# Optimization experiments

Measured on AMD Instinct MI355X. Metric: run time of the kernel, lower is better.

Reference implementation:

```python
import jax, jax.numpy as jnp
import numpy as np

B, T, I = 16384, 101, 4
H = 512  # lstm_hidden_layer_size
M = 512  # mlp_hidden_layer_size


def setup_inputs() -> dict:
    key = jax.random.key(0)
    ks = jax.random.split(key, 10)
    s_ih = 1.0 / np.sqrt(H)
    inp = {
        "batch_x": jax.random.normal(ks[0], (B, T, I), dtype=jnp.float32),
        "batch_a": jax.random.uniform(ks[1], (B, 1), dtype=jnp.float32),
        # PyTorch nn.LSTM params (gate order i,f,g,o), U(-1/sqrt(H), 1/sqrt(H))
        "W_ih": jax.random.uniform(ks[2], (4 * H, I), minval=-s_ih, maxval=s_ih, dtype=jnp.float32),
        "W_hh": jax.random.uniform(ks[3], (4 * H, H), minval=-s_ih, maxval=s_ih, dtype=jnp.float32),
        "b_ih": jax.random.uniform(ks[4], (4 * H,), minval=-s_ih, maxval=s_ih, dtype=jnp.float32),
        "b_hh": jax.random.uniform(ks[5], (4 * H,), minval=-s_ih, maxval=s_ih, dtype=jnp.float32),
        "W1": jax.random.uniform(ks[6], (M, H), minval=-s_ih, maxval=s_ih, dtype=jnp.float32),
        "b1": jax.random.uniform(ks[7], (M,), minval=-s_ih, maxval=s_ih, dtype=jnp.float32),
        "W2": jax.random.uniform(ks[8], (1, M + 1), minval=-1.0 / np.sqrt(M + 1), maxval=1.0 / np.sqrt(M + 1), dtype=jnp.float32),
        "b2": jax.random.uniform(ks[9], (1,), minval=-1.0 / np.sqrt(M + 1), maxval=1.0 / np.sqrt(M + 1), dtype=jnp.float32),
    }
    return inp


def _lstm_last_hidden(batch_x, W_ih, W_hh, b_ih, b_hh):
    h = W_hh.shape[1]
    # input projections for all timesteps at once: [T, B, 4H]
    x_proj = jnp.einsum("bti,gi->tbg", batch_x, W_ih) + b_ih + b_hh

    def step(carry, xp):
        h_t, c_t = carry
        gates = xp + h_t @ W_hh.T  # [B, 4H]
        i, f, g, o = jnp.split(gates, 4, axis=-1)
        i = jax.nn.sigmoid(i)
        f = jax.nn.sigmoid(f)
        g = jnp.tanh(g)
        o = jax.nn.sigmoid(o)
        c_new = f * c_t + i * g
        h_new = o * jnp.tanh(c_new)
        return (h_new, c_new), None

    b = batch_x.shape[0]
    h0 = jnp.zeros((b, h), dtype=batch_x.dtype)
    c0 = jnp.zeros((b, h), dtype=batch_x.dtype)
    (h_T, _), _ = jax.lax.scan(step, (h0, c0), x_proj)
    return h_T  # [B, H]


def reference(batch_x, batch_a, W_ih, W_hh, b_ih, b_hh, W1, b1, W2, b2):
    h_T = _lstm_last_hidden(batch_x, W_ih, W_hh, b_ih, b_hh)
    x = jax.nn.relu(h_T @ W1.T + b1)
    # dropout(p=0.3) treated as identity (eval-mode) for a deterministic reference
    x = jnp.concatenate([x, batch_a], axis=1)  # [B, M+1]
    return x @ W2.T + b2  # [B, 1]
```

## Files before the change

### kernel.cpp

```cpp
#include <hip/hip_runtime.h>
#include <hip/hip_bf16.h>

#define BATCH 16384
#define TSTEPS 101
#define HDIM 512
#define GDIM 2048

typedef __attribute__((ext_vector_type(8))) short s16x8;
typedef __attribute__((ext_vector_type(16))) float f32x16;
typedef __attribute__((ext_vector_type(4))) float f32x4;

__device__ __forceinline__ float sigm(float x){ return 1.0f/(1.0f + __expf(-x)); }
__device__ __forceinline__ float tanhx(float x){ float e=__expf(2.0f*x); return 1.0f - 2.0f/(e+1.0f); }

__device__ __forceinline__ void gload16(const void* g, void* l){
  __builtin_amdgcn_global_load_lds((const __attribute__((address_space(1))) unsigned int*)g,
                                   (__attribute__((address_space(3))) unsigned int*)l, 16, 0, 0);
}

__global__ __launch_bounds__(512, 2) void lstm_step(
    const __hip_bfloat16* __restrict__ hin,
    __hip_bfloat16* __restrict__ hout,
    float* __restrict__ cbuf,
    const float* __restrict__ bx,
    const float* __restrict__ Wih,
    const float* __restrict__ bcomb,
    const __hip_bfloat16* __restrict__ wbf,
    int t, int skipmm)
{
  __shared__ short sA[256*64];
  __shared__ short sB[256*64];
  const int tid = threadIdx.x;
  const int l  = tid & 63, w = tid >> 6;
  const int lo = l & 31,  hi = l >> 5;
  const int wr = w >> 1,  wc = w & 1;

  const int orig = blockIdx.x;
  const int swz = (orig & 7)*64 + (orig >> 3);
  const int panel = swz >> 3;
  const int cq    = swz & 7;

  f32x16 acc[4][2] = {};

  if (!skipmm){
    const __hip_bfloat16* asrc[4]; int adst[4];
    const __hip_bfloat16* bsrc[4]; int bdst[4];
    #pragma unroll
    for (int i = 0; i < 4; ++i){
      int c = i*512 + tid;
      int row = c >> 3, s = c & 7;
      int kc = s ^ (row & 7);
      asrc[i] = hin + (size_t)(panel*256 + row)*HDIM + kc*8;
      adst[i] = c*8;
      int g = row >> 6, hcw = row & 63;
      bsrc[i] = wbf + (size_t)(g*HDIM + cq*64 + hcw)*HDIM + kc*8;
      bdst[i] = c*8;
    }
    const int xorv = (lo & 7);
    const int rowA0 = wr*64 + lo, rowA1 = rowA0 + 32;

    for (int kt = 0; kt < 8; ++kt){
      const int k0 = kt*64;
      __syncthreads();
      #pragma unroll
      for (int i = 0; i < 4; ++i) gload16(asrc[i] + k0, &sA[adst[i]]);
      #pragma unroll
      for (int i = 0; i < 4; ++i) gload16(bsrc[i] + k0, &sB[bdst[i]]);
      __syncthreads();
      #pragma unroll
      for (int kk = 0; kk < 4; ++kk){
        const int so = ((kk*2 + hi) ^ xorv) * 8;
        s16x8 av0 = *(const s16x8*)&sA[rowA0*64 + so];
        s16x8 av1 = *(const s16x8*)&sA[rowA1*64 + so];
        #pragma unroll
        for (int g = 0; g < 4; ++g){
          s16x8 bv = *(const s16x8*)&sB[(g*64 + wc*32 + lo)*64 + so];
          acc[g][0] = __builtin_amdgcn_mfma_f32_32x32x16_bf16(av0, bv, acc[g][0], 0, 0, 0);
          acc[g][1] = __builtin_amdgcn_mfma_f32_32x32x16_bf16(av1, bv, acc[g][1], 0, 0, 0);
        }
      }
    }
  }

  const int colg = cq*64 + wc*32 + lo;
  float4 wv[4]; float bc4[4];
  #pragma unroll
  for (int g = 0; g < 4; ++g){
    int gc = g*HDIM + colg;
    wv[g]  = *(const float4*)(Wih + (size_t)gc*4);
    bc4[g] = bcomb[gc];
  }
  #pragma unroll
  for (int m = 0; m < 2; ++m){
    #pragma unroll
    for (int q = 0; q < 4; ++q){
      #pragma unroll
      for (int i2 = 0; i2 < 4; ++i2){
        const int reg = q*4 + i2;
        const int r = panel*256 + wr*64 + m*32 + q*8 + hi*4 + i2;
        float4 xv = *(const float4*)(bx + ((size_t)r*TSTEPS + t)*4);
        float pi = acc[0][m][reg] + bc4[0] + xv.x*wv[0].x + xv.y*wv[0].y + xv.z*wv[0].z + xv.w*wv[0].w;
        float pf = acc[1][m][reg] + bc4[1] + xv.x*wv[1].x + xv.y*wv[1].y + xv.z*wv[1].z + xv.w*wv[1].w;
        float pg = acc[2][m][reg] + bc4[2] + xv.x*wv[2].x + xv.y*wv[2].y + xv.z*wv[2].z + xv.w*wv[2].w;
        float po = acc[3][m][reg] + bc4[3] + xv.x*wv[3].x + xv.y*wv[3].y + xv.z*wv[3].z + xv.w*wv[3].w;
        float iv = sigm(pi), fv = sigm(pf), gv = tanhx(pg), ov = sigm(po);
        size_t idx = (size_t)r*HDIM + colg;
        float cold = skipmm ? 0.f : cbuf[idx];
        float cn = fv*cold + iv*gv;
        cbuf[idx] = cn;
        hout[idx] = __float2bfloat16(ov*tanhx(cn));
      }
    }
  }
}

__global__ void prep(const float* __restrict__ Whh, const float* __restrict__ W1,
                     const float* __restrict__ bih, const float* __restrict__ bhh,
                     __hip_bfloat16* __restrict__ wbf, __hip_bfloat16* __restrict__ w1bf,
                     float* __restrict__ bcomb){
  int i = blockIdx.x*256 + threadIdx.x;
  if (i < GDIM*HDIM) wbf[i] = __float2bfloat16(Whh[i]);
  if (i < HDIM*HDIM) w1bf[i] = __float2bfloat16(W1[i]);
  if (i < GDIM) bcomb[i] = bih[i] + bhh[i];
}

__global__ __launch_bounds__(256) void mlp1(const __hip_bfloat16* __restrict__ hT,
                                            const __hip_bfloat16* __restrict__ w1bf,
                                            const float* __restrict__ b1, float* __restrict__ xout){
  __shared__ short sA[128*64];
  __shared__ short sB[128*64];
  const int tid = threadIdx.x;
  const int l = tid & 63, w = tid >> 6;
  const int lr = l & 15, lk = l >> 4;
  const int r0 = blockIdx.x * 128, c0 = blockIdx.y * 128;

  f32x4 acc[2][8] = {};
  for (int k0 = 0; k0 < HDIM; k0 += 64){
    __syncthreads();
    #pragma unroll
    for (int i = 0; i < 4; ++i){
      int cch = i*256 + tid;
      int row = cch >> 3, kc = cch & 7;
      int kcs = kc ^ (row & 7);
      gload16(hT + (size_t)(r0 + row)*HDIM + k0 + kcs*8, &sA[cch*8]);
    }
    #pragma unroll
    for (int i = 0; i < 4; ++i){
      int cch = i*256 + tid;
      int row = cch >> 3, kc = cch & 7;
      int kcs = kc ^ (row & 7);
      gload16(w1bf + (size_t)(c0 + row)*HDIM + k0 + kcs*8, &sB[cch*8]);
    }
    __syncthreads();
    #pragma unroll
    for (int kk = 0; kk < 2; ++kk){
      s16x8 av[2];
      #pragma unroll
      for (int m = 0; m < 2; ++m){
        int row = w*32 + m*16 + lr;
        int slot = row*8 + ((kk*4 + lk) ^ (row & 7));
        av[m] = *(const s16x8*)&sA[slot*8];
      }
      #pragma unroll
      for (int n = 0; n < 8; ++n){
        int rB = n*16 + lr;
        int slot = rB*8 + ((kk*4 + lk) ^ (rB & 7));
        s16x8 bv = *(const s16x8*)&sB[slot*8];
        #pragma unroll
        for (int m = 0; m < 2; ++m)
          acc[m][n] = __builtin_amdgcn_mfma_f32_16x16x32_bf16(av[m], bv, acc[m][n], 0, 0, 0);
      }
    }
  }
  #pragma unroll
  for (int m = 0; m < 2; ++m){
    #pragma unroll
    for (int rg = 0; rg < 4; ++rg){
      int r = r0 + w*32 + m*16 + lk*4 + rg;
      #pragma unroll
      for (int n = 0; n < 8; ++n){
        int c = c0 + n*16 + lr;
        float v = acc[m][n][rg] + b1[c];
        xout[(size_t)r*HDIM + c] = v > 0.f ? v : 0.f;
      }
    }
  }
}

__global__ __launch_bounds__(256) void mlp2(const float* __restrict__ x, const float* __restrict__ a,
                                            const float* __restrict__ W2, const float* __restrict__ b2,
                                            float* __restrict__ out){
  const int wi = threadIdx.x >> 6, l = threadIdx.x & 63;
  const int b = blockIdx.x*4 + wi;
  const float* xr = x + (size_t)b*HDIM;
  float4 v0 = *(const float4*)(xr + l*8);
  float4 v1 = *(const float4*)(xr + l*8 + 4);
  float4 w0 = *(const float4*)(W2 + l*8);
  float4 w1 = *(const float4*)(W2 + l*8 + 4);
  float s = v0.x*w0.x + v0.y*w0.y + v0.z*w0.z + v0.w*w0.w
          + v1.x*w1.x + v1.y*w1.y + v1.z*w1.z + v1.w*w1.w;
  #pragma unroll
  for (int off = 32; off > 0; off >>= 1) s += __shfl_down(s, off);
  if (l == 0) out[b] = s + a[b]*W2[HDIM] + b2[0];
}

extern "C" void kernel_launch(void* const* d_in, const int* in_sizes, int n_in,
                              void* d_out, int out_size, void* d_ws, size_t ws_size,
                              hipStream_t stream){
  const float* bx  = (const float*)d_in[0];
  const float* ba  = (const float*)d_in[1];
  const float* Wih = (const float*)d_in[2];
  const float* Whh = (const float*)d_in[3];
  const float* bih = (const float*)d_in[4];
  const float* bhh = (const float*)d_in[5];
  const float* W1  = (const float*)d_in[6];
  const float* b1  = (const float*)d_in[7];
  const float* W2  = (const float*)d_in[8];
  const float* b2  = (const float*)d_in[9];
  float* out = (float*)d_out;

  char* ws = (char*)d_ws;
  __hip_bfloat16* wbf   = (__hip_bfloat16*)(ws);
  __hip_bfloat16* w1bf  = (__hip_bfloat16*)(ws + 2097152);
  float*          bcomb = (float*)(ws + 2621440);
  __hip_bfloat16* hb0   = (__hip_bfloat16*)(ws + 2629632);
  __hip_bfloat16* hb1   = (__hip_bfloat16*)(ws + 19406848);
  float*          cbuf  = (float*)(ws + 36184064);
  float*          xmlp  = cbuf;

  prep<<<4096, 256, 0, stream>>>(Whh, W1, bih, bhh, wbf, w1bf, bcomb);

  for (int t = 0; t < TSTEPS; ++t){
    const __hip_bfloat16* hin = (t & 1) ? hb1 : hb0;
    __hip_bfloat16*      hout = (t & 1) ? hb0 : hb1;
    lstm_step<<<512, 512, 0, stream>>>(hin, hout, cbuf, bx, Wih, bcomb, wbf,
                                       t, (t == 0) ? 1 : 0);
  }
  mlp1<<<dim3(128, 4), 256, 0, stream>>>(hb1, w1bf, b1, xmlp);
  mlp2<<<4096, 256, 0, stream>>>(xmlp, ba, W2, b2, out);
}
```

Measured before the change: 7.040 ms.

## Retile LSTM step GEMM to 256x128 tiles with 16x16x32 MFMA

Each block now handles a 256-row batch panel against 32 hidden columns (128 gate columns), using 256 threads and 1024 blocks instead of 512 threads and 512 blocks. The inner product switches from 32x32x16 to 16x16x32 bf16 MFMA, and each warp covers 128 rows times 16 columns per gate. The B tile in LDS is halved, so more blocks can fit per CU and each A fragment is reused across more MFMAs. In exchange the accumulator count per thread rises (32 f32x4), which raises register pressure, and the h panel is reloaded by twice as many blocks.

```diff
diff --git a/kernel.cpp b/kernel.cpp
--- a/kernel.cpp
+++ b/kernel.cpp
@@ -7,7 +7,6 @@
 #define GDIM 2048
 
 typedef __attribute__((ext_vector_type(8))) short s16x8;
-typedef __attribute__((ext_vector_type(16))) float f32x16;
 typedef __attribute__((ext_vector_type(4))) float f32x4;
 
 __device__ __forceinline__ float sigm(float x){ return 1.0f/(1.0f + __expf(-x)); }
@@ -18,7 +17,7 @@
                                    (__attribute__((address_space(3))) unsigned int*)l, 16, 0, 0);
 }
 
-__global__ __launch_bounds__(512, 2) void lstm_step(
+__global__ __launch_bounds__(256, 2) void lstm_step(
     const __hip_bfloat16* __restrict__ hin,
     __hip_bfloat16* __restrict__ hout,
     float* __restrict__ cbuf,
@@ -29,60 +28,71 @@
     int t, int skipmm)
 {
   __shared__ short sA[256*64];
-  __shared__ short sB[256*64];
+  __shared__ short sB[128*64];
   const int tid = threadIdx.x;
-  const int l  = tid & 63, w = tid >> 6;
-  const int lo = l & 31,  hi = l >> 5;
-  const int wr = w >> 1,  wc = w & 1;
+  const int l = tid & 63, w = tid >> 6;
+  const int lr = l & 15, lk = l >> 4;
+  const int wr = w >> 1, wc = w & 1;
 
   const int orig = blockIdx.x;
-  const int swz = (orig & 7)*64 + (orig >> 3);
-  const int panel = swz >> 3;
-  const int cq    = swz & 7;
-
-  f32x16 acc[4][2] = {};
+  const int swz = (orig & 7)*128 + (orig >> 3);
+  const int panel = swz >> 4;
+  const int cb    = swz & 15;
+
+  f32x4 acc[4][8] = {};
 
   if (!skipmm){
-    const __hip_bfloat16* asrc[4]; int adst[4];
-    const __hip_bfloat16* bsrc[4]; int bdst[4];
-    #pragma unroll
-    for (int i = 0; i < 4; ++i){
-      int c = i*512 + tid;
+    const __hip_bfloat16* asrc[8]; int adst[8];
+    #pragma unroll
+    for (int i = 0; i < 8; ++i){
+      int c = i*256 + tid;
       int row = c >> 3, s = c & 7;
       int kc = s ^ (row & 7);
       asrc[i] = hin + (size_t)(panel*256 + row)*HDIM + kc*8;
       adst[i] = c*8;
-      int g = row >> 6, hcw = row & 63;
-      bsrc[i] = wbf + (size_t)(g*HDIM + cq*64 + hcw)*HDIM + kc*8;
+    }
+    const __hip_bfloat16* bsrc[4]; int bdst[4];
+    #pragma unroll
+    for (int i = 0; i < 4; ++i){
+      int c = i*256 + tid;
+      int row = c >> 3, s = c & 7;
+      int kc = s ^ (row & 7);
+      int g = row >> 5, hcw = row & 31;
+      bsrc[i] = wbf + (size_t)(g*HDIM + cb*32 + hcw)*HDIM + kc*8;
       bdst[i] = c*8;
     }
-    const int xorv = (lo & 7);
-    const int rowA0 = wr*64 + lo, rowA1 = rowA0 + 32;
 
     for (int kt = 0; kt < 8; ++kt){
       const int k0 = kt*64;
       __syncthreads();
       #pragma unroll
-      for (int i = 0; i < 4; ++i) gload16(asrc[i] + k0, &sA[adst[i]]);
+      for (int i = 0; i < 8; ++i) gload16(asrc[i] + k0, &sA[adst[i]]);
       #pragma unroll
       for (int i = 0; i < 4; ++i) gload16(bsrc[i] + k0, &sB[bdst[i]]);
       __syncthreads();
       #pragma unroll
-      for (int kk = 0; kk < 4; ++kk){
-        const int so = ((kk*2 + hi) ^ xorv) * 8;
-        s16x8 av0 = *(const s16x8*)&sA[rowA0*64 + so];
-        s16x8 av1 = *(const s16x8*)&sA[rowA1*64 + so];
+      for (int kk = 0; kk < 2; ++kk){
+        s16x8 av[8];
+        #pragma unroll
+        for (int m = 0; m < 8; ++m){
+          int row = wr*128 + m*16 + lr;
+          int slot = row*8 + ((kk*4 + lk) ^ (row & 7));
+          av[m] = *(const s16x8*)&sA[slot*8];
+        }
         #pragma unroll
         for (int g = 0; g < 4; ++g){
-          s16x8 bv = *(const s16x8*)&sB[(g*64 + wc*32 + lo)*64 + so];
-          acc[g][0] = __builtin_amdgcn_mfma_f32_32x32x16_bf16(av0, bv, acc[g][0], 0, 0, 0);
-          acc[g][1] = __builtin_amdgcn_mfma_f32_32x32x16_bf16(av1, bv, acc[g][1], 0, 0, 0);
+          int rB = g*32 + wc*16 + lr;
+          int slot = rB*8 + ((kk*4 + lk) ^ (rB & 7));
+          s16x8 bv = *(const s16x8*)&sB[slot*8];
+          #pragma unroll
+          for (int m = 0; m < 8; ++m)
+            acc[g][m] = __builtin_amdgcn_mfma_f32_16x16x32_bf16(av[m], bv, acc[g][m], 0, 0, 0);
         }
       }
     }
   }
 
-  const int colg = cq*64 + wc*32 + lo;
+  const int colg = cb*32 + wc*16 + lr;
   float4 wv[4]; float bc4[4];
   #pragma unroll
   for (int g = 0; g < 4; ++g){
@@ -91,25 +101,21 @@
     bc4[g] = bcomb[gc];
   }
   #pragma unroll
-  for (int m = 0; m < 2; ++m){
-    #pragma unroll
-    for (int q = 0; q < 4; ++q){
-      #pragma unroll
-      for (int i2 = 0; i2 < 4; ++i2){
-        const int reg = q*4 + i2;
-        const int r = panel*256 + wr*64 + m*32 + q*8 + hi*4 + i2;
-        float4 xv = *(const float4*)(bx + ((size_t)r*TSTEPS + t)*4);
-        float pi = acc[0][m][reg] + bc4[0] + xv.x*wv[0].x + xv.y*wv[0].y + xv.z*wv[0].z + xv.w*wv[0].w;
-        float pf = acc[1][m][reg] + bc4[1] + xv.x*wv[1].x + xv.y*wv[1].y + xv.z*wv[1].z + xv.w*wv[1].w;
-        float pg = acc[2][m][reg] + bc4[2] + xv.x*wv[2].x + xv.y*wv[2].y + xv.z*wv[2].z + xv.w*wv[2].w;
-        float po = acc[3][m][reg] + bc4[3] + xv.x*wv[3].x + xv.y*wv[3].y + xv.z*wv[3].z + xv.w*wv[3].w;
-        float iv = sigm(pi), fv = sigm(pf), gv = tanhx(pg), ov = sigm(po);
-        size_t idx = (size_t)r*HDIM + colg;
-        float cold = skipmm ? 0.f : cbuf[idx];
-        float cn = fv*cold + iv*gv;
-        cbuf[idx] = cn;
-        hout[idx] = __float2bfloat16(ov*tanhx(cn));
-      }
+  for (int m = 0; m < 8; ++m){
+    #pragma unroll
+    for (int rg = 0; rg < 4; ++rg){
+      int r = panel*256 + wr*128 + m*16 + lk*4 + rg;
+      float4 xv = *(const float4*)(bx + ((size_t)r*TSTEPS + t)*4);
+      float pi = acc[0][m][rg] + bc4[0] + xv.x*wv[0].x + xv.y*wv[0].y + xv.z*wv[0].z + xv.w*wv[0].w;
+      float pf = acc[1][m][rg] + bc4[1] + xv.x*wv[1].x + xv.y*wv[1].y + xv.z*wv[1].z + xv.w*wv[1].w;
+      float pg = acc[2][m][rg] + bc4[2] + xv.x*wv[2].x + xv.y*wv[2].y + xv.z*wv[2].z + xv.w*wv[2].w;
+      float po = acc[3][m][rg] + bc4[3] + xv.x*wv[3].x + xv.y*wv[3].y + xv.z*wv[3].z + xv.w*wv[3].w;
+      float iv = sigm(pi), fv = sigm(pf), gv = tanhx(pg), ov = sigm(po);
+      size_t idx = (size_t)r*HDIM + colg;
+      float cold = skipmm ? 0.f : cbuf[idx];
+      float cn = fv*cold + iv*gv;
+      cbuf[idx] = cn;
+      hout[idx] = __float2bfloat16(ov*tanhx(cn));
     }
   }
 }
@@ -233,8 +239,8 @@
   for (int t = 0; t < TSTEPS; ++t){
     const __hip_bfloat16* hin = (t & 1) ? hb1 : hb0;
     __hip_bfloat16*      hout = (t & 1) ? hb0 : hb1;
-    lstm_step<<<512, 512, 0, stream>>>(hin, hout, cbuf, bx, Wih, bcomb, wbf,
-                                       t, (t == 0) ? 1 : 0);
+    lstm_step<<<1024, 256, 0, stream>>>(hin, hout, cbuf, bx, Wih, bcomb, wbf,
+                                        t, (t == 0) ? 1 : 0);
   }
   mlp1<<<dim3(128, 4), 256, 0, stream>>>(hb1, w1bf, b1, xmlp);
   mlp2<<<4096, 256, 0, stream>>>(xmlp, ba, W2, b2, out);
```

Result: faster. 6.597 ms (-6.3%).
